# Performance work log

Hardware: AMD Instinct MI355X
Metric: run time of the kernel (lower is better)

## Reference

```python
import jax, jax.numpy as jnp
import numpy as np

VOCAB, EMB, HID = 5000, 16, 32
B, T = 256, 2048


def setup_inputs() -> dict:
    key = jax.random.key(0)
    k1, k2, k3, k4, k5 = jax.random.split(key, 5)
    tokens = jax.random.randint(k1, (B, T), 0, VOCAB, dtype=jnp.int32)
    emb = jax.random.normal(k2, (VOCAB, EMB), dtype=jnp.float32) * 0.05
    Wk = jax.random.normal(k3, (EMB, 4 * HID), dtype=jnp.float32) * 0.1
    Wr = jax.random.normal(k4, (HID, 4 * HID), dtype=jnp.float32) * 0.1
    b = jax.random.normal(k5, (4 * HID,), dtype=jnp.float32) * 0.1
    return {"tokens": tokens, "emb": emb, "Wk": Wk, "Wr": Wr, "b": b}


def reference(tokens, emb, Wk, Wr, b):
    # Embedding lookup: [B, T, EMB]
    x = emb[tokens]
    # Mask: Keras Masking on tiled token values -> masked where token == 0.
    mask = (tokens != 0)  # [B, T] True = valid step
    # Precompute input projections for all timesteps: [B, T, 4H]
    zx = jnp.einsum('bte,eh->bth', x, Wk) + b
    zx_t = jnp.swapaxes(zx, 0, 1)        # [T, B, 4H]
    mask_t = jnp.swapaxes(mask, 0, 1)    # [T, B]

    def step(carry, inp):
        h, c = carry
        z_x, m = inp
        z = z_x + h @ Wr                      # [B, 4H]
        i, f, g, o = jnp.split(z, 4, axis=-1) # Keras gate order i,f,g,o
        i = jax.nn.sigmoid(i)
        f = jax.nn.sigmoid(f)
        g = jnp.tanh(g)
        o = jax.nn.sigmoid(o)
        c_new = f * c + i * g
        h_new = o * jnp.tanh(c_new)
        m = m[:, None]
        # Keras masked RNN: masked steps carry forward previous state/output
        h = jnp.where(m, h_new, h)
        c = jnp.where(m, c_new, c)
        return (h, c), h

    h0 = jnp.zeros((tokens.shape[0], HID), dtype=zx.dtype)
    c0 = jnp.zeros((tokens.shape[0], HID), dtype=zx.dtype)
    _, hs = jax.lax.scan(step, (h0, c0), (zx_t, mask_t))
    return jnp.swapaxes(hs, 0, 1)  # [B, T, HID]
```

## Files before the change

kernel.cpp:

```cpp
#include <hip/hip_runtime.h>

#define G    128
#define HID  32
#define EMB  16
#define BB   256
#define TT   2048
#define VOC  5000

#define LOG2E      1.44269504088896340736f
#define NEG2LOG2E -2.88539008177792681472f

typedef float v2f __attribute__((ext_vector_type(2)));
typedef __attribute__((ext_vector_type(8))) short short8;
typedef __attribute__((ext_vector_type(4))) float f32x4;

__device__ __forceinline__ float bf2f(unsigned short u) {
    return __uint_as_float(((unsigned)u) << 16);
}
__device__ __forceinline__ unsigned short f2bf(float f) {
    unsigned x = __float_as_uint(f);
    return (unsigned short)((x + 0x7FFFu + ((x >> 16) & 1u)) >> 16);
}
__device__ __forceinline__ float sigm2(float x) {
    const float e = __builtin_amdgcn_exp2f(-x);
    return __builtin_amdgcn_rcpf(1.f + e);
}
__device__ __forceinline__ float tanh_n(float x) {
    const float e = __builtin_amdgcn_exp2f(x * NEG2LOG2E);
    return (1.f - e) * __builtin_amdgcn_rcpf(1.f + e);
}
__device__ __forceinline__ float sigm(float x) {
    const float e = __expf(-x);
    return __builtin_amdgcn_rcpf(1.f + e);
}
__device__ __forceinline__ float tanh_f(float x) {
    const float e = __expf(-2.f * x);
    return (1.f - e) * __builtin_amdgcn_rcpf(1.f + e);
}
__device__ __forceinline__ float rdlf(float v, int k) {
    return __int_as_float(__builtin_amdgcn_readlane(__float_as_int(v), k));
}
template <int CTRL>
__device__ __forceinline__ unsigned dppq_u(unsigned v) {
    return (unsigned)__builtin_amdgcn_update_dpp(0, (int)v, CTRL, 0xF, 0xF, true);
}
template <int CTRL>
__device__ __forceinline__ float dppq_f(float v) {
    return __uint_as_float(dppq_u<CTRL>(__float_as_uint(v)));
}
#define DPP_XOR1   0xB1
#define DPP_XOR2   0x4E
#define DPP_HMIRR  0x141
#define DPP_ROR8   0x128
#define DPP_MIRR   0x140

__device__ __host__ __forceinline__ int col_a(int l) {
    return (l >> 1) + 32 * (l & 1);
}

__global__ __launch_bounds__(64) void detect_kernel(
    const unsigned int* __restrict__ bias_w, int* __restrict__ flag)
{
    const int l = threadIdx.x;
    const unsigned u  = bias_w[l];
    const unsigned lo = u & 0xFFFFu;
    const float vlo = __uint_as_float(lo << 16);
    const float vhi = __uint_as_float(u & 0xFFFF0000u);
    const bool nz_even = (lo != 0u);
    const bool big = !(fabsf(vlo) < 1e6f) || !(fabsf(vhi) < 1e6f);
    const unsigned long long nz = __ballot(nz_even);
    const unsigned long long bg = __ballot(big);
    if (l == 0 && blockIdx.x == 0)
        *flag = (nz == 0ull || bg != 0ull) ? 1 : 0;
}

__global__ __launch_bounds__(64) void zk_kernel(
    const void* __restrict__ emb, const void* __restrict__ Wk,
    const void* __restrict__ bias, float* __restrict__ ZK,
    const int* __restrict__ flag)
{
    const int l = threadIdx.x;
    const int v = blockIdx.x;
    const bool f32 = flag[0] != 0;
    const int ca = col_a(l), cb = ca + 64;

    float x[EMB], wa[EMB], wb[EMB], ba, bb;
    if (f32) {
        const float* E = (const float*)emb + (size_t)v * EMB;
        const float* W = (const float*)Wk;
        const float* B = (const float*)bias;
#pragma unroll
        for (int e = 0; e < EMB; ++e) {
            x[e]  = E[e];
            wa[e] = W[e * G + ca];
            wb[e] = W[e * G + cb];
        }
        ba = B[ca]; bb = B[cb];
    } else {
        const unsigned short* E = (const unsigned short*)emb + (size_t)v * EMB;
        const unsigned short* W = (const unsigned short*)Wk;
        const unsigned short* B = (const unsigned short*)bias;
#pragma unroll
        for (int e = 0; e < EMB; ++e) {
            x[e]  = bf2f(E[e]);
            wa[e] = bf2f(W[e * G + ca]);
            wb[e] = bf2f(W[e * G + cb]);
        }
        ba = bf2f(B[ca]); bb = bf2f(B[cb]);
    }
    float za = ba, zb = bb;
#pragma unroll
    for (int e = 0; e < EMB; ++e) {
        za = fmaf(x[e], wa[e], za);
        zb = fmaf(x[e], wb[e], zb);
    }
    ZK[(size_t)v * G + 2 * l]     = za * LOG2E;
    ZK[(size_t)v * G + 2 * l + 1] = zb * LOG2E;
}

template <bool F32OUT>
__device__ __forceinline__ void scan_zk_loop(
    const int* __restrict__ trow, const float* __restrict__ ZK,
    void* __restrict__ orow, const short8 (&Bf)[8], int lane)
{
    const bool  h0  = (lane & 1) == 0;
    const float zsc = h0 ? 2.f : 1.f, gm = h0 ? 2.f : 1.f, ga = h0 ? -1.f : 0.f;
    const int   oj  = lane >> 1;
    const int   g4  = (lane >> 4) & 3;
    const bool  u_odd = (lane >> 1) & 1;

    const f32x4 zc = {0.f, 0.f, 0.f, 0.f};
    float h = 0.f, c = 0.f;

    int tcur[16], tnxt[16];
#pragma unroll
    for (int p = 0; p < 16; ++p) tcur[p] = trow[p];
#pragma unroll
    for (int p = 0; p < 16; ++p) tnxt[p] = trow[16 + p];

    v2f pz[4];
#pragma unroll
    for (int d = 0; d < 4; ++d)
        pz[d] = *(const v2f*)(ZK + (size_t)tcur[d] * G + 2 * lane);

    for (int cc = 0; cc < TT / 16; ++cc) {
        const int base = cc * 16;
#pragma unroll
        for (int u = 0; u < 16; ++u) {
            const int t = base + u;
            const v2f z = pz[u & 3];
            {
                const int ptok = (u + 4 < 16) ? tcur[u + 4] : tnxt[u + 4 - 16];
                pz[u & 3] = *(const v2f*)(ZK + (size_t)ptok * G + 2 * lane);
            }

            const unsigned rh  = __float_as_uint(h) + 0x8000u;
            const unsigned prt = dppq_u<DPP_XOR2>(rh);
            const unsigned plo = u_odd ? prt : rh;
            const unsigned phi = u_odd ? rh : prt;
            const unsigned pair = __builtin_amdgcn_perm(phi, plo, 0x07060302u);
            const unsigned q1 = dppq_u<DPP_HMIRR>(pair);
            const unsigned q2 = dppq_u<DPP_ROR8 >(pair);
            const unsigned q3 = dppq_u<DPP_MIRR >(pair);
            union { unsigned u4[4]; short8 s8; } au;
            au.u4[0] = pair; au.u4[1] = q1; au.u4[2] = q2; au.u4[3] = q3;
            const short8 Af = au.s8;

            f32x4 d0 = __builtin_amdgcn_mfma_f32_16x16x32_bf16(Af, Bf[0], zc, 0, 0, 0);
            f32x4 d1 = __builtin_amdgcn_mfma_f32_16x16x32_bf16(Af, Bf[1], zc, 0, 0, 0);
            f32x4 d2 = __builtin_amdgcn_mfma_f32_16x16x32_bf16(Af, Bf[2], zc, 0, 0, 0);
            f32x4 d3 = __builtin_amdgcn_mfma_f32_16x16x32_bf16(Af, Bf[3], zc, 0, 0, 0);
            f32x4 d4 = __builtin_amdgcn_mfma_f32_16x16x32_bf16(Af, Bf[4], zc, 0, 0, 0);
            f32x4 d5 = __builtin_amdgcn_mfma_f32_16x16x32_bf16(Af, Bf[5], zc, 0, 0, 0);
            f32x4 d6 = __builtin_amdgcn_mfma_f32_16x16x32_bf16(Af, Bf[6], zc, 0, 0, 0);
            f32x4 d7 = __builtin_amdgcn_mfma_f32_16x16x32_bf16(Af, Bf[7], zc, 0, 0, 0);

            const float mva = (g4 < 2) ? (g4 == 0 ? d0.x : d1.x)
                                       : (g4 == 2 ? d2.x : d3.x);
            const float mvb = (g4 < 2) ? (g4 == 0 ? d4.x : d5.x)
                                       : (g4 == 2 ? d6.x : d7.x);
            const float za = z.x + mva;
            const float zb = z.y + mvb;

            const float aa1 = sigm2(za);
            const float s2  = sigm2(zb * zsc);
            const float aa2 = fmaf(s2, gm, ga);
            const float x1  = dppq_f<DPP_XOR1>(aa1);
            const float x2  = dppq_f<DPP_XOR1>(aa2);
            const float iV = h0 ? aa1 : x1, fV = h0 ? x1 : aa1;
            const float gV = h0 ? aa2 : x2, oV = h0 ? x2 : aa2;
            const float cN = fmaf(fV, c, iV * gV);
            const float hN = oV * tanh_n(cN);
            const bool  m  = tcur[u] != 0;
            c = m ? cN : c;
            h = m ? hN : h;

            const int oi = t * HID + oj;
            if (F32OUT) __builtin_nontemporal_store(h, (float*)orow + oi);
            else        __builtin_nontemporal_store(f2bf(h), (unsigned short*)orow + oi);
        }
#pragma unroll
        for (int p = 0; p < 16; ++p) tcur[p] = tnxt[p];
        const int nb = (cc + 2) * 16;
        if (nb <= TT - 16) {
#pragma unroll
            for (int p = 0; p < 16; ++p) tnxt[p] = trow[nb + p];
        }
    }
}

__global__ __launch_bounds__(64) void scan_zk_kernel(
    const int* __restrict__ tokens, const float* __restrict__ ZK,
    const void* __restrict__ Wr, const void* __restrict__ bias,
    void* __restrict__ out, const int* __restrict__ flag)
{
    const int lane = threadIdx.x, b = blockIdx.x;
    const bool f32 = flag[0] != 0;

    short8 Bf[8];
    const int n  = lane & 15;
    const int k0 = (lane >> 4) * 8;
#pragma unroll
    for (int p = 0; p < 8; ++p) {
        const int ell = 16 * (p & 3) + n;
        const int col = (p < 4) ? col_a(ell) : (col_a(ell) + 64);
        const int jx  = (p & 3) << 1;
        short el[8];
        if (f32) {
            const float* W = (const float*)Wr;
#pragma unroll
            for (int j = 0; j < 8; ++j)
                el[j] = (short)f2bf(W[(k0 + (j ^ jx)) * G + col] * LOG2E);
        } else {
            const unsigned short* W = (const unsigned short*)Wr;
#pragma unroll
            for (int j = 0; j < 8; ++j)
                el[j] = (short)f2bf(bf2f(W[(k0 + (j ^ jx)) * G + col]) * LOG2E);
        }
        short8 s;
#pragma unroll
        for (int j = 0; j < 8; ++j) s[j] = el[j];
        Bf[p] = s;
    }

    const int* trow = tokens + (size_t)b * TT;
    if (f32) scan_zk_loop<true >(trow, ZK, (char*)out + (size_t)b * TT * HID * 4, Bf, lane);
    else     scan_zk_loop<false>(trow, ZK, (char*)out + (size_t)b * TT * HID * 2, Bf, lane);
}

template <bool F32>
__device__ __forceinline__ void row_load(const void* emb, int tok, uint4* r) {
    if (F32) { const uint4* p = (const uint4*)((const float*)emb + (size_t)tok*EMB);
               r[0]=p[0]; r[1]=p[1]; r[2]=p[2]; r[3]=p[3]; }
    else     { const uint4* p = (const uint4*)((const unsigned short*)emb + (size_t)tok*EMB);
               r[0]=p[0]; r[1]=p[1]; }
}
template <bool F32>
__device__ __forceinline__ void row_unpack(const uint4* r, float* x) {
    if (F32) {
        const unsigned w[16] = {r[0].x,r[0].y,r[0].z,r[0].w, r[1].x,r[1].y,r[1].z,r[1].w,
                                r[2].x,r[2].y,r[2].z,r[2].w, r[3].x,r[3].y,r[3].z,r[3].w};
#pragma unroll
        for (int e = 0; e < 16; ++e) x[e] = __uint_as_float(w[e]);
    } else {
        const unsigned w[8] = {r[0].x,r[0].y,r[0].z,r[0].w, r[1].x,r[1].y,r[1].z,r[1].w};
#pragma unroll
        for (int q = 0; q < 8; ++q) {
            x[2*q]   = __uint_as_float(w[q] << 16);
            x[2*q+1] = __uint_as_float(w[q] & 0xFFFF0000u);
        }
    }
}

template <bool F32>
__device__ __forceinline__ void scan_fused_loop(
    const int* __restrict__ trow, const void* __restrict__ emb, void* orow,
    const float (&wka)[EMB], const float (&wkb)[EMB],
    const float (&wra)[HID], const float (&wrb)[HID],
    float za0, float zb0, const int* tl, int lane)
{
    const bool  lo  = lane < HID;
    const float zsc = lo ? 2.f : 1.f, gm = lo ? 2.f : 1.f, ga = lo ? -1.f : 0.f;
    float h = 0.f, c = 0.f;
    uint4 praw[2][4];
    row_load<F32>(emb, trow[0], praw[0]);
    row_load<F32>(emb, trow[1], praw[1]);

    for (int tt = 0; tt < TT; tt += 2) {
#pragma unroll
        for (int u = 0; u < 2; ++u) {
            const int t = tt + u;
            float x[EMB];
            row_unpack<F32>(praw[u], x);
            int tn = t + 2; tn = tn > TT - 1 ? TT - 1 : tn;
            row_load<F32>(emb, tl[tn], praw[u]);
            float za = za0, zb = zb0;
#pragma unroll
            for (int e = 0; e < EMB; ++e) { za = fmaf(x[e], wka[e], za); zb = fmaf(x[e], wkb[e], zb); }
#pragma unroll
            for (int k = 0; k < HID; ++k) {
                const float hk = rdlf(h, k);
                za = fmaf(hk, wra[k], za);
                zb = fmaf(hk, wrb[k], zb);
            }
            const float a1 = sigm(za);
            const float s2 = sigm(zb * zsc);
            const float a2 = fmaf(s2, gm, ga);
            const float x1 = __shfl_xor(a1, 32);
            const float x2 = __shfl_xor(a2, 32);
            const float iV = lo ? a1 : x1, fV = lo ? x1 : a1;
            const float gV = lo ? a2 : x2, oV = lo ? x2 : a2;
            const float cN = fmaf(fV, c, iV * gV);
            const float hN = oV * tanh_f(cN);
            const bool  m  = tl[t] != 0;
            c = m ? cN : c;
            h = m ? hN : h;
            const int oi = t * HID + (lane & (HID - 1));
            if (F32) ((float*)orow)[oi] = h;
            else     ((unsigned short*)orow)[oi] = f2bf(h);
        }
    }
}

__global__ __launch_bounds__(64) void scan_fused_kernel(
    const int* __restrict__ tokens, const void* __restrict__ emb,
    const void* __restrict__ Wk, const void* __restrict__ Wr,
    const void* __restrict__ bias, void* __restrict__ out,
    const int* __restrict__ flag, int defmode)
{
    __shared__ int tl[TT];
    const int lane = threadIdx.x, b = blockIdx.x;
    const bool f32 = flag ? (flag[0] != 0) : (defmode != 0);
    const int* trow = tokens + (size_t)b * TT;
    for (int t = lane; t < TT; t += 64) tl[t] = trow[t];

    float wka[EMB], wkb[EMB], wra[HID], wrb[HID], za0, zb0;
    if (f32) {
        const float* WK = (const float*)Wk; const float* WR = (const float*)Wr;
        const float* B  = (const float*)bias;
#pragma unroll
        for (int e = 0; e < EMB; ++e) { wka[e] = WK[e*G + lane]; wkb[e] = WK[e*G + lane + 64]; }
#pragma unroll
        for (int k = 0; k < HID; ++k) { wra[k] = WR[k*G + lane]; wrb[k] = WR[k*G + lane + 64]; }
        za0 = B[lane]; zb0 = B[lane + 64];
    } else {
        const unsigned short* WK = (const unsigned short*)Wk;
        const unsigned short* WR = (const unsigned short*)Wr;
        const unsigned short* B  = (const unsigned short*)bias;
#pragma unroll
        for (int e = 0; e < EMB; ++e) { wka[e] = bf2f(WK[e*G + lane]); wkb[e] = bf2f(WK[e*G + lane + 64]); }
#pragma unroll
        for (int k = 0; k < HID; ++k) { wra[k] = bf2f(WR[k*G + lane]); wrb[k] = bf2f(WR[k*G + lane + 64]); }
        za0 = bf2f(B[lane]); zb0 = bf2f(B[lane + 64]);
    }
    __syncthreads();

    if (f32) scan_fused_loop<true >(trow, emb, (char*)out + (size_t)b*TT*HID*4,
                                    wka, wkb, wra, wrb, za0, zb0, tl, lane);
    else     scan_fused_loop<false>(trow, emb, (char*)out + (size_t)b*TT*HID*2,
                                    wka, wkb, wra, wrb, za0, zb0, tl, lane);
}

extern "C" void kernel_launch(void* const* d_in, const int* in_sizes, int n_in,
                              void* d_out, int out_size, void* d_ws, size_t ws_size,
                              hipStream_t stream) {
    const int*  tokens = (const int*)d_in[0];
    const void* emb    = d_in[1];
    const void* Wk     = d_in[2];
    const void* Wr     = d_in[3];
    const void* bias   = d_in[4];

    const size_t zk_off   = 256;
    const size_t zk_bytes = (size_t)VOC * G * sizeof(float);

    if (ws_size >= zk_off + zk_bytes) {
        int*   flag = (int*)d_ws;
        float* ZK   = (float*)((char*)d_ws + zk_off);
        detect_kernel<<<1, 64, 0, stream>>>((const unsigned int*)bias, flag);
        zk_kernel<<<VOC, 64, 0, stream>>>(emb, Wk, bias, ZK, flag);
        scan_zk_kernel<<<BB, 64, 0, stream>>>(tokens, ZK, Wr, bias, d_out, flag);
    } else if (ws_size >= 16) {
        int* flag = (int*)d_ws;
        detect_kernel<<<1, 64, 0, stream>>>((const unsigned int*)bias, flag);
        scan_fused_kernel<<<BB, 64, 0, stream>>>(tokens, emb, Wk, Wr, bias, d_out, flag, 1);
    } else {
        scan_fused_kernel<<<BB, 64, 0, stream>>>(tokens, emb, Wk, Wr, bias, d_out, nullptr, 1);
    }
}
```

Before: 439.6 us.

## Shorten LSTM recurrence critical path and batch ZK rows per block

Folds the 2x tanh pre-scale for the g gate into the ZK table and the recurrent weights, so the per-step multiply disappears. Replaces the two XOR1 DPP swaps and selects with row-broadcast DPPs and a fused i*g product, and computes o*tanh(c) through a single exp2/rcp form. Token loads are now coalesced per lane and spread with readlane, and ZK prefetch depth goes from 4 to 8 steps. The ZK kernel handles 8 vocab rows per block so the Wk loads are reused across rows. This relies on VOC being divisible by 8 and on the new DPP broadcast patterns matching the gate layout.

```diff
diff --git a/kernel.cpp b/kernel.cpp
--- a/kernel.cpp
+++ b/kernel.cpp
@@ -8,7 +8,7 @@
 #define VOC  5000
 
 #define LOG2E      1.44269504088896340736f
-#define NEG2LOG2E -2.88539008177792681472f
+#define TWOLOG2E   2.88539008177792681472f
 
 typedef float v2f __attribute__((ext_vector_type(2)));
 typedef __attribute__((ext_vector_type(8))) short short8;
@@ -25,10 +25,6 @@
     const float e = __builtin_amdgcn_exp2f(-x);
     return __builtin_amdgcn_rcpf(1.f + e);
 }
-__device__ __forceinline__ float tanh_n(float x) {
-    const float e = __builtin_amdgcn_exp2f(x * NEG2LOG2E);
-    return (1.f - e) * __builtin_amdgcn_rcpf(1.f + e);
-}
 __device__ __forceinline__ float sigm(float x) {
     const float e = __expf(-x);
     return __builtin_amdgcn_rcpf(1.f + e);
@@ -48,8 +44,9 @@
 __device__ __forceinline__ float dppq_f(float v) {
     return __uint_as_float(dppq_u<CTRL>(__float_as_uint(v)));
 }
-#define DPP_XOR1   0xB1
 #define DPP_XOR2   0x4E
+#define DPP_BODD   0xF5
+#define DPP_BEVN   0xA0
 #define DPP_HMIRR  0x141
 #define DPP_ROR8   0x128
 #define DPP_MIRR   0x140
@@ -74,48 +71,56 @@
         *flag = (nz == 0ull || bg != 0ull) ? 1 : 0;
 }
 
+#define ZK_RPB 8
 __global__ __launch_bounds__(64) void zk_kernel(
     const void* __restrict__ emb, const void* __restrict__ Wk,
     const void* __restrict__ bias, float* __restrict__ ZK,
     const int* __restrict__ flag)
 {
-    const int l = threadIdx.x;
-    const int v = blockIdx.x;
+    const int l  = threadIdx.x;
+    const int v0 = blockIdx.x * ZK_RPB;
     const bool f32 = flag[0] != 0;
     const int ca = col_a(l), cb = ca + 64;
-
-    float x[EMB], wa[EMB], wb[EMB], ba, bb;
+    const float sa = LOG2E;
+    const float sb = ((l & 1) == 0) ? 2.f * LOG2E : LOG2E;
+
+    float wa[EMB], wb[EMB], ba, bb;
     if (f32) {
-        const float* E = (const float*)emb + (size_t)v * EMB;
         const float* W = (const float*)Wk;
         const float* B = (const float*)bias;
 #pragma unroll
-        for (int e = 0; e < EMB; ++e) {
-            x[e]  = E[e];
-            wa[e] = W[e * G + ca];
-            wb[e] = W[e * G + cb];
-        }
+        for (int e = 0; e < EMB; ++e) { wa[e] = W[e * G + ca]; wb[e] = W[e * G + cb]; }
         ba = B[ca]; bb = B[cb];
     } else {
-        const unsigned short* E = (const unsigned short*)emb + (size_t)v * EMB;
         const unsigned short* W = (const unsigned short*)Wk;
         const unsigned short* B = (const unsigned short*)bias;
 #pragma unroll
+        for (int e = 0; e < EMB; ++e) { wa[e] = bf2f(W[e * G + ca]); wb[e] = bf2f(W[e * G + cb]); }
+        ba = bf2f(B[ca]); bb = bf2f(B[cb]);
+    }
+
+#pragma unroll
+    for (int r = 0; r < ZK_RPB; ++r) {
+        const int v = v0 + r;
+        float x[EMB];
+        if (f32) {
+            const float* E = (const float*)emb + (size_t)v * EMB;
+#pragma unroll
+            for (int e = 0; e < EMB; ++e) x[e] = E[e];
+        } else {
+            const unsigned short* E = (const unsigned short*)emb + (size_t)v * EMB;
+#pragma unroll
+            for (int e = 0; e < EMB; ++e) x[e] = bf2f(E[e]);
+        }
+        float za = ba, zb = bb;
+#pragma unroll
         for (int e = 0; e < EMB; ++e) {
-            x[e]  = bf2f(E[e]);
-            wa[e] = bf2f(W[e * G + ca]);
-            wb[e] = bf2f(W[e * G + cb]);
-        }
-        ba = bf2f(B[ca]); bb = bf2f(B[cb]);
-    }
-    float za = ba, zb = bb;
-#pragma unroll
-    for (int e = 0; e < EMB; ++e) {
-        za = fmaf(x[e], wa[e], za);
-        zb = fmaf(x[e], wb[e], zb);
-    }
-    ZK[(size_t)v * G + 2 * l]     = za * LOG2E;
-    ZK[(size_t)v * G + 2 * l + 1] = zb * LOG2E;
+            za = fmaf(x[e], wa[e], za);
+            zb = fmaf(x[e], wb[e], zb);
+        }
+        ZK[(size_t)v * G + 2 * l]     = za * sa;
+        ZK[(size_t)v * G + 2 * l + 1] = zb * sb;
+    }
 }
 
 template <bool F32OUT>
@@ -124,41 +129,45 @@
     void* __restrict__ orow, const short8 (&Bf)[8], int lane)
 {
     const bool  h0  = (lane & 1) == 0;
-    const float zsc = h0 ? 2.f : 1.f, gm = h0 ? 2.f : 1.f, ga = h0 ? -1.f : 0.f;
+    const float gm  = h0 ? 2.f : 1.f, ga = h0 ? -1.f : 0.f;
     const int   oj  = lane >> 1;
     const int   g4  = (lane >> 4) & 3;
     const bool  u_odd = (lane >> 1) & 1;
+    const unsigned psel = u_odd ? 0x03020706u : 0x07060302u;
+    const int   lm  = lane & 15;
 
     const f32x4 zc = {0.f, 0.f, 0.f, 0.f};
     float h = 0.f, c = 0.f;
 
-    int tcur[16], tnxt[16];
-#pragma unroll
-    for (int p = 0; p < 16; ++p) tcur[p] = trow[p];
-#pragma unroll
-    for (int p = 0; p < 16; ++p) tnxt[p] = trow[16 + p];
-
-    v2f pz[4];
-#pragma unroll
-    for (int d = 0; d < 4; ++d)
-        pz[d] = *(const v2f*)(ZK + (size_t)tcur[d] * G + 2 * lane);
+    int tva = trow[lm];
+    int tvb = trow[16 + lm];
+    int tc[16], tn[16];
+#pragma unroll
+    for (int p = 0; p < 16; ++p) tc[p] = __builtin_amdgcn_readlane(tva, p);
+#pragma unroll
+    for (int p = 0; p < 16; ++p) tn[p] = __builtin_amdgcn_readlane(tvb, p);
+
+    v2f pz[8];
+#pragma unroll
+    for (int d = 0; d < 8; ++d)
+        pz[d] = *(const v2f*)(ZK + (size_t)tc[d] * G + 2 * lane);
 
     for (int cc = 0; cc < TT / 16; ++cc) {
         const int base = cc * 16;
+        const int nxtc = (cc + 2 < TT / 16) ? (cc + 2) : (TT / 16 - 1);
+        const int tvc = trow[nxtc * 16 + lm];
 #pragma unroll
         for (int u = 0; u < 16; ++u) {
             const int t = base + u;
-            const v2f z = pz[u & 3];
+            const v2f z = pz[u & 7];
             {
-                const int ptok = (u + 4 < 16) ? tcur[u + 4] : tnxt[u + 4 - 16];
-                pz[u & 3] = *(const v2f*)(ZK + (size_t)ptok * G + 2 * lane);
+                const int ptok = (u + 8 < 16) ? tc[u + 8] : tn[u - 8];
+                pz[u & 7] = *(const v2f*)(ZK + (size_t)ptok * G + 2 * lane);
             }
 
             const unsigned rh  = __float_as_uint(h) + 0x8000u;
             const unsigned prt = dppq_u<DPP_XOR2>(rh);
-            const unsigned plo = u_odd ? prt : rh;
-            const unsigned phi = u_odd ? rh : prt;
-            const unsigned pair = __builtin_amdgcn_perm(phi, plo, 0x07060302u);
+            const unsigned pair = __builtin_amdgcn_perm(prt, rh, psel);
             const unsigned q1 = dppq_u<DPP_HMIRR>(pair);
             const unsigned q2 = dppq_u<DPP_ROR8 >(pair);
             const unsigned q3 = dppq_u<DPP_MIRR >(pair);
@@ -183,15 +192,21 @@
             const float zb = z.y + mvb;
 
             const float aa1 = sigm2(za);
-            const float s2  = sigm2(zb * zsc);
-            const float aa2 = fmaf(s2, gm, ga);
-            const float x1  = dppq_f<DPP_XOR1>(aa1);
-            const float x2  = dppq_f<DPP_XOR1>(aa2);
-            const float iV = h0 ? aa1 : x1, fV = h0 ? x1 : aa1;
-            const float gV = h0 ? aa2 : x2, oV = h0 ? x2 : aa2;
-            const float cN = fmaf(fV, c, iV * gV);
-            const float hN = oV * tanh_n(cN);
-            const bool  m  = tcur[u] != 0;
+            const float s2  = sigm2(zb);
+            const float aam = aa1 * gm;
+            const float qc  = aa1 * ga;
+            const float q   = fmaf(aam, s2, qc);
+            const float fG  = dppq_f<DPP_BODD>(aa1);
+            const float oG  = dppq_f<DPP_BODD>(s2);
+            const float pr  = dppq_f<DPP_BEVN>(q);
+            const float cN  = fmaf(fG, c, pr);
+
+            const float ex = __builtin_amdgcn_exp2f(cN * TWOLOG2E);
+            const float rr = __builtin_amdgcn_rcpf(ex + 1.f);
+            const float oo = oG + oG;
+            const float hN = fmaf(-oo, rr, oG);
+
+            const bool m = tc[u] != 0;
             c = m ? cN : c;
             h = m ? hN : h;
 
@@ -200,12 +215,9 @@
             else        __builtin_nontemporal_store(f2bf(h), (unsigned short*)orow + oi);
         }
 #pragma unroll
-        for (int p = 0; p < 16; ++p) tcur[p] = tnxt[p];
-        const int nb = (cc + 2) * 16;
-        if (nb <= TT - 16) {
-#pragma unroll
-            for (int p = 0; p < 16; ++p) tnxt[p] = trow[nb + p];
-        }
+        for (int p = 0; p < 16; ++p) tc[p] = tn[p];
+#pragma unroll
+        for (int p = 0; p < 16; ++p) tn[p] = __builtin_amdgcn_readlane(tvc, p);
     }
 }
 
@@ -225,17 +237,18 @@
         const int ell = 16 * (p & 3) + n;
         const int col = (p < 4) ? col_a(ell) : (col_a(ell) + 64);
         const int jx  = (p & 3) << 1;
+        const float sc = (p >= 4 && (n & 1) == 0) ? 2.f * LOG2E : LOG2E;
         short el[8];
         if (f32) {
             const float* W = (const float*)Wr;
 #pragma unroll
             for (int j = 0; j < 8; ++j)
-                el[j] = (short)f2bf(W[(k0 + (j ^ jx)) * G + col] * LOG2E);
+                el[j] = (short)f2bf(W[(k0 + (j ^ jx)) * G + col] * sc);
         } else {
             const unsigned short* W = (const unsigned short*)Wr;
 #pragma unroll
             for (int j = 0; j < 8; ++j)
-                el[j] = (short)f2bf(bf2f(W[(k0 + (j ^ jx)) * G + col]) * LOG2E);
+                el[j] = (short)f2bf(bf2f(W[(k0 + (j ^ jx)) * G + col]) * sc);
         }
         short8 s;
 #pragma unroll
@@ -377,7 +390,7 @@
         int*   flag = (int*)d_ws;
         float* ZK   = (float*)((char*)d_ws + zk_off);
         detect_kernel<<<1, 64, 0, stream>>>((const unsigned int*)bias, flag);
-        zk_kernel<<<VOC, 64, 0, stream>>>(emb, Wk, bias, ZK, flag);
+        zk_kernel<<<VOC / ZK_RPB, 64, 0, stream>>>(emb, Wk, bias, ZK, flag);
         scan_zk_kernel<<<BB, 64, 0, stream>>>(tokens, ZK, Wr, bias, d_out, flag);
     } else if (ws_size >= 16) {
         int* flag = (int*)d_ws;
```

Result: no change. 441.4 us (+0.4%).
